# Kernel tuning notes

Measured on AMD Instinct MI355X. Metric: run time of the kernel, lower is better.

Reference implementation:

```python
import jax, jax.numpy as jnp
import numpy as np

SEQ, BATCH, IN, HID = 2048, 64, 256, 256


def setup_inputs() -> dict:
    key = jax.random.key(0)
    ks = jax.random.split(key, 9)
    s_in = 1.0 / np.sqrt(IN)
    s_h = 1.0 / np.sqrt(HID)
    return {
        "x": jax.random.normal(ks[0], (SEQ, BATCH, IN), dtype=jnp.float32),
        "hidden": jnp.zeros((BATCH, HID), dtype=jnp.float32),
        # torch nn.Linear params: weight (out, in), bias (out,)
        "Wz": jax.random.uniform(ks[1], (HID, IN), jnp.float32, -s_in, s_in),
        "bz": jax.random.uniform(ks[2], (HID,), jnp.float32, -s_in, s_in),
        "Uz": jax.random.uniform(ks[3], (HID, HID), jnp.float32, -s_h, s_h),
        "cz": jax.random.uniform(ks[4], (HID,), jnp.float32, -s_h, s_h),
        "Wh": jax.random.uniform(ks[5], (HID, IN), jnp.float32, -s_in, s_in),
        "bh": jax.random.uniform(ks[6], (HID,), jnp.float32, -s_in, s_in),
        "Uh": jax.random.uniform(ks[7], (HID, HID), jnp.float32, -s_h, s_h),
        "ch": jax.random.uniform(ks[8], (HID,), jnp.float32, -s_h, s_h),
    }


def reference(x, hidden, Wz, bz, Uz, cz, Wh, bh, Uh, ch):
    # Precompute all input projections in two batched GEMMs: (S,B,I)@(I,H)
    xz = jnp.einsum("sbi,hi->sbh", x, Wz) + bz  # W_z x_t + b_z
    xh = jnp.einsum("sbi,hi->sbh", x, Wh) + bh  # W_h x_t + b_h

    def step(h, inp):
        xz_t, xh_t = inp
        z = jax.nn.sigmoid(xz_t + h @ Uz.T + cz)
        h_tilde = jnp.tanh(xh_t + h @ Uh.T + ch)
        h_new = (1.0 - z) * h + z * h_tilde
        return h_new, h_new

    h_final, outputs = jax.lax.scan(step, hidden, (xz, xh))
    return outputs, h_final
```

## Files before the change

### kernel.cpp

```cpp
#include <hip/hip_runtime.h>
#include <math.h>

#define SEQ   2048
#define BATCH 64
#define IN    256
#define HID   256
#define NBLK  (SEQ / 8)

typedef _Float16 hf2 __attribute__((ext_vector_type(2)));
typedef _Float16 hf4 __attribute__((ext_vector_type(4)));
typedef _Float16 hf8 __attribute__((ext_vector_type(8)));
typedef float    f32x4 __attribute__((ext_vector_type(4)));

static __device__ __forceinline__ float fast_sigmoid(float x) {
    return __builtin_amdgcn_rcpf(1.0f + __expf(-x));
}

static __device__ __forceinline__ float fast_tanh(float x) {
    const float e = __expf(-2.0f * x);
    return fmaf(2.0f, __builtin_amdgcn_rcpf(1.0f + e), -1.0f);
}

static __device__ __forceinline__ hf8 cvt8(const float4& a, const float4& b) {
    hf8 f;
    f[0] = (_Float16)a.x; f[1] = (_Float16)a.y;
    f[2] = (_Float16)a.z; f[3] = (_Float16)a.w;
    f[4] = (_Float16)b.x; f[5] = (_Float16)b.y;
    f[6] = (_Float16)b.z; f[7] = (_Float16)b.w;
    return f;
}

static __device__ __forceinline__ void bar_lds() {
    asm volatile("s_waitcnt lgkmcnt(0)" ::: "memory");
    __builtin_amdgcn_s_barrier();
}

__global__ __launch_bounds__(256) void w16_kernel(
    const float* __restrict__ Wz, const float* __restrict__ Wh,
    _Float16* __restrict__ W16)
{
    const int idx = blockIdx.x * 256 + threadIdx.x;
    const int row = idx >> 8;
    const int col = idx & 255;
    const float v = (row < 256) ? Wz[row * 256 + col] : Wh[(row - 256) * 256 + col];
    W16[idx] = (_Float16)v;
}

__global__ __launch_bounds__(256) void proj_mfma_kernel(
    const float* __restrict__ x,
    const _Float16* __restrict__ W16,
    const float* __restrict__ bz, const float* __restrict__ cz,
    const float* __restrict__ bh, const float* __restrict__ ch,
    _Float16* __restrict__ xz16,
    float* __restrict__ xh_out)
{
    const int tid  = threadIdx.x;
    const int lane = tid & 63;
    const int w    = tid >> 6;
    const int m0   = blockIdx.x * 16;
    const int col0 = w * 128;

    const int r = lane & 15;
    const int g = lane >> 4;

    f32x4 acc[8] = {f32x4{0,0,0,0}, f32x4{0,0,0,0}, f32x4{0,0,0,0}, f32x4{0,0,0,0},
                    f32x4{0,0,0,0}, f32x4{0,0,0,0}, f32x4{0,0,0,0}, f32x4{0,0,0,0}};

    const float*    xrow  = x   + (size_t)(m0 + r) * IN + g * 8;
    const _Float16* wbase = W16 + (size_t)(col0 + r) * IN + g * 8;

#pragma unroll
    for (int kt = 0; kt < 8; ++kt) {
        const float4 xa = *reinterpret_cast<const float4*>(xrow + kt * 32);
        const float4 xb = *reinterpret_cast<const float4*>(xrow + kt * 32 + 4);
        const hf8 a = cvt8(xa, xb);
#pragma unroll
        for (int t = 0; t < 8; ++t) {
            const hf8 bfrag = *reinterpret_cast<const hf8*>(
                wbase + (size_t)t * 16 * IN + kt * 32);
            acc[t] = __builtin_amdgcn_mfma_f32_16x16x32_f16(a, bfrag, acc[t], 0, 0, 0);
        }
    }

    if (w < 2) {
#pragma unroll
        for (int t = 0; t < 8; ++t) {
            const int c = col0 + t * 16 + r;
            const float bsum = bz[c] + cz[c];
#pragma unroll
            for (int reg = 0; reg < 4; ++reg) {
                const int m = m0 + 4 * g + reg;
                xz16[(size_t)m * HID + c] = (_Float16)(acc[t][reg] + bsum);
            }
        }
    } else {
#pragma unroll
        for (int t = 0; t < 8; ++t) {
            const int c = col0 - 256 + t * 16 + r;
            const float bsum = bh[c] + ch[c];
#pragma unroll
            for (int reg = 0; reg < 4; ++reg) {
                const int m = m0 + 4 * g + reg;
                xh_out[(size_t)m * HID + c] = acc[t][reg] + bsum;
            }
        }
    }
}

__global__ __launch_bounds__(512, 2) void rec_mfma_kernel(
    const float* __restrict__ hidden0,
    const float* __restrict__ Uz,
    const float* __restrict__ Uh,
    const _Float16* __restrict__ xz16,
    float* __restrict__ out,
    float* __restrict__ h_final)
{
    const int b    = blockIdx.x;
    const int tid  = threadIdx.x;
    const int w    = tid >> 6;
    const int lane = tid & 63;
    const int r    = lane & 15;
    const int g    = lane >> 4;

    __shared__ __align__(16) _Float16 hbuf[2][256];
    __shared__ __align__(16) float    sbuf[8][64];
    __shared__ __align__(16) _Float16 xzs[2][8][256];
    __shared__ __align__(16) float    xhs[2][8][256];

    hf8 au[4][8];
    {
        const float* usrc = (r & 1) ? Uh : Uz;
        const int    hrow = r >> 1;
#pragma unroll
        for (int i = 0; i < 4; ++i) {
            const int m = 4 * w + i;
            const float* p0 = usrc + (size_t)(8 * m + hrow) * HID;
#pragma unroll
            for (int kt = 0; kt < 8; ++kt) {
                const float* p = p0 + kt * 32 + 8 * g;
                au[i][kt] = cvt8(*reinterpret_cast<const float4*>(p),
                                 *reinterpret_cast<const float4*>(p + 4));
            }
        }
    }

    if (tid < 256) {
        hbuf[0][tid] = (_Float16)hidden0[b * HID + tid];
    }

    const int o = 32 * w + lane;
    float hp = 0.0f;
    float* pst = out + (size_t)b * HID + o;
    if (lane < 32) {
        hp = hidden0[b * HID + o];
    }

    const int srow = tid >> 6;
    const int scol = (tid & 63) * 4;
    hf4   rz;
    f32x4 rh;
    {
        const size_t a0 = ((size_t)srow * BATCH + b) * HID + scol;
        const hf4   z0 = *reinterpret_cast<const hf4*>(xz16 + a0);
        const f32x4 h0 = *reinterpret_cast<const f32x4*>(out + a0);
        *reinterpret_cast<hf4*>(&xzs[0][srow][scol])   = z0;
        *reinterpret_cast<f32x4*>(&xhs[0][srow][scol]) = h0;
        const size_t a1 = ((size_t)(8 + srow) * BATCH + b) * HID + scol;
        rz = *reinterpret_cast<const hf4*>(xz16 + a1);
        rh = *reinterpret_cast<const f32x4*>(out + a1);
    }
    __syncthreads();

    for (int j = 0; j < NBLK; ++j) {
        const int jb = j & 1;
#pragma unroll
        for (int s = 0; s < 8; ++s) {
            float xzc = 0.0f, xhc = 0.0f;
            if (lane < 32) {
                xzc = (float)xzs[jb][s][o];
                xhc = xhs[jb][s][o];
            }
            hf8 bb[8];
#pragma unroll
            for (int kt = 0; kt < 8; ++kt) {
                bb[kt] = *reinterpret_cast<const hf8*>(
                    &hbuf[s & 1][kt * 32 + 8 * g]);
            }
            f32x4 acc[4] = {f32x4{0,0,0,0}, f32x4{0,0,0,0},
                            f32x4{0,0,0,0}, f32x4{0,0,0,0}};
#pragma unroll
            for (int kt = 0; kt < 8; ++kt) {
#pragma unroll
                for (int i = 0; i < 4; ++i) {
                    acc[i] = __builtin_amdgcn_mfma_f32_16x16x32_f16(
                        au[i][kt], bb[kt], acc[i], 0, 0, 0);
                }
            }
            if (r == 0) {
#pragma unroll
                for (int i = 0; i < 4; ++i) {
                    *reinterpret_cast<f32x4*>(&sbuf[w][i * 16 + g * 4]) = acc[i];
                }
            }
            if (lane < 32) {
                const float2 pr = *reinterpret_cast<const float2*>(
                    &sbuf[w][2 * lane]);
                const float z  = fast_sigmoid(pr.x + xzc);
                const float th = fast_tanh(pr.y + xhc);
                hp = fmaf(z, th - hp, hp);
                *pst = hp;
                pst += (size_t)BATCH * HID;
                hbuf[(s + 1) & 1][o] = (_Float16)hp;
            }
            if (s == 7 && j + 1 < NBLK) {
                *reinterpret_cast<hf4*>(&xzs[jb ^ 1][srow][scol])   = rz;
                *reinterpret_cast<f32x4*>(&xhs[jb ^ 1][srow][scol]) = rh;
                int trow = 8 * (j + 2) + srow;
                if (trow >= SEQ) trow = SEQ - 1;
                const size_t an = ((size_t)trow * BATCH + b) * HID + scol;
                rz = *reinterpret_cast<const hf4*>(xz16 + an);
                rh = *reinterpret_cast<const f32x4*>(out + an);
            }
            bar_lds();
        }
    }

    if (lane < 32) {
        h_final[(size_t)b * HID + o] = hp;
    }
}

extern "C" void kernel_launch(void* const* d_in, const int* in_sizes, int n_in,
                              void* d_out, int out_size, void* d_ws, size_t ws_size,
                              hipStream_t stream) {
    const float* x      = (const float*)d_in[0];
    const float* hidden = (const float*)d_in[1];
    const float* Wz     = (const float*)d_in[2];
    const float* bz     = (const float*)d_in[3];
    const float* Uz     = (const float*)d_in[4];
    const float* cz     = (const float*)d_in[5];
    const float* Wh     = (const float*)d_in[6];
    const float* bh     = (const float*)d_in[7];
    const float* Uh     = (const float*)d_in[8];
    const float* ch     = (const float*)d_in[9];

    float* out     = (float*)d_out;
    float* h_final = out + (size_t)SEQ * BATCH * HID;

    _Float16* xz16 = (_Float16*)d_ws;
    _Float16* W16  = (_Float16*)((char*)d_ws + ((size_t)64 << 20));

    w16_kernel<<<512, 256, 0, stream>>>(Wz, Wh, W16);

    proj_mfma_kernel<<<(SEQ * BATCH) / 16, 256, 0, stream>>>(
        x, W16, bz, cz, bh, ch, xz16, out);

    rec_mfma_kernel<<<BATCH, 512, 0, stream>>>(
        hidden, Uz, Uh, xz16, out, h_final);
}
```

Before: 2.163 ms.

## Split recurrent step across 16 waves with two MFMA tiles each

The recurrent kernel now launches 1024 threads (16 waves) per batch row instead of 512, so each wave owns two 16-row U tiles rather than four. This halves the serial MFMA chain per time step and the per-wave register footprint for the U fragments, and it shortens the critical path of each sequential step. The cost is more waves in each per-step barrier and fewer lanes per wave doing the gate math, which makes barrier synchronisation more expensive.

Result: faster. 2.081 ms (-3.8%).

```diff
diff --git a/kernel.cpp b/kernel.cpp
--- a/kernel.cpp
+++ b/kernel.cpp
@@ -10,6 +10,7 @@
 typedef _Float16 hf2 __attribute__((ext_vector_type(2)));
 typedef _Float16 hf4 __attribute__((ext_vector_type(4)));
 typedef _Float16 hf8 __attribute__((ext_vector_type(8)));
+typedef float    f32x2 __attribute__((ext_vector_type(2)));
 typedef float    f32x4 __attribute__((ext_vector_type(4)));
 
 static __device__ __forceinline__ float fast_sigmoid(float x) {
@@ -107,7 +108,7 @@
     }
 }
 
-__global__ __launch_bounds__(512, 2) void rec_mfma_kernel(
+__global__ __launch_bounds__(1024, 1) void rec_mfma_kernel(
     const float* __restrict__ hidden0,
     const float* __restrict__ Uz,
     const float* __restrict__ Uh,
@@ -123,17 +124,17 @@
     const int g    = lane >> 4;
 
     __shared__ __align__(16) _Float16 hbuf[2][256];
-    __shared__ __align__(16) float    sbuf[8][64];
+    __shared__ __align__(16) float    sbuf[512];
     __shared__ __align__(16) _Float16 xzs[2][8][256];
     __shared__ __align__(16) float    xhs[2][8][256];
 
-    hf8 au[4][8];
+    hf8 au[2][8];
     {
         const float* usrc = (r & 1) ? Uh : Uz;
         const int    hrow = r >> 1;
 #pragma unroll
-        for (int i = 0; i < 4; ++i) {
-            const int m = 4 * w + i;
+        for (int i = 0; i < 2; ++i) {
+            const int m = 2 * w + i;
             const float* p0 = usrc + (size_t)(8 * m + hrow) * HID;
 #pragma unroll
             for (int kt = 0; kt < 8; ++kt) {
@@ -148,26 +149,26 @@
         hbuf[0][tid] = (_Float16)hidden0[b * HID + tid];
     }
 
-    const int o = 32 * w + lane;
+    const int o = 16 * w + (lane & 15);
     float hp = 0.0f;
     float* pst = out + (size_t)b * HID + o;
-    if (lane < 32) {
+    if (lane < 16) {
         hp = hidden0[b * HID + o];
     }
 
-    const int srow = tid >> 6;
-    const int scol = (tid & 63) * 4;
-    hf4   rz;
-    f32x4 rh;
+    const int srow = tid >> 7;
+    const int scol = (tid & 127) * 2;
+    hf2   rz;
+    f32x2 rh;
     {
         const size_t a0 = ((size_t)srow * BATCH + b) * HID + scol;
-        const hf4   z0 = *reinterpret_cast<const hf4*>(xz16 + a0);
-        const f32x4 h0 = *reinterpret_cast<const f32x4*>(out + a0);
-        *reinterpret_cast<hf4*>(&xzs[0][srow][scol])   = z0;
-        *reinterpret_cast<f32x4*>(&xhs[0][srow][scol]) = h0;
+        *reinterpret_cast<hf2*>(&xzs[0][srow][scol]) =
+            *reinterpret_cast<const hf2*>(xz16 + a0);
+        *reinterpret_cast<f32x2*>(&xhs[0][srow][scol]) =
+            *reinterpret_cast<const f32x2*>(out + a0);
         const size_t a1 = ((size_t)(8 + srow) * BATCH + b) * HID + scol;
-        rz = *reinterpret_cast<const hf4*>(xz16 + a1);
-        rh = *reinterpret_cast<const f32x4*>(out + a1);
+        rz = *reinterpret_cast<const hf2*>(xz16 + a1);
+        rh = *reinterpret_cast<const f32x2*>(out + a1);
     }
     __syncthreads();
 
@@ -176,56 +177,47 @@
 #pragma unroll
         for (int s = 0; s < 8; ++s) {
             float xzc = 0.0f, xhc = 0.0f;
-            if (lane < 32) {
+            if (lane < 16) {
                 xzc = (float)xzs[jb][s][o];
                 xhc = xhs[jb][s][o];
             }
-            hf8 bb[8];
+            f32x4 acc0{0, 0, 0, 0}, acc1{0, 0, 0, 0};
 #pragma unroll
             for (int kt = 0; kt < 8; ++kt) {
-                bb[kt] = *reinterpret_cast<const hf8*>(
+                const hf8 bb = *reinterpret_cast<const hf8*>(
                     &hbuf[s & 1][kt * 32 + 8 * g]);
-            }
-            f32x4 acc[4] = {f32x4{0,0,0,0}, f32x4{0,0,0,0},
-                            f32x4{0,0,0,0}, f32x4{0,0,0,0}};
-#pragma unroll
-            for (int kt = 0; kt < 8; ++kt) {
-#pragma unroll
-                for (int i = 0; i < 4; ++i) {
-                    acc[i] = __builtin_amdgcn_mfma_f32_16x16x32_f16(
-                        au[i][kt], bb[kt], acc[i], 0, 0, 0);
-                }
+                acc0 = __builtin_amdgcn_mfma_f32_16x16x32_f16(
+                    au[0][kt], bb, acc0, 0, 0, 0);
+                acc1 = __builtin_amdgcn_mfma_f32_16x16x32_f16(
+                    au[1][kt], bb, acc1, 0, 0, 0);
             }
             if (r == 0) {
-#pragma unroll
-                for (int i = 0; i < 4; ++i) {
-                    *reinterpret_cast<f32x4*>(&sbuf[w][i * 16 + g * 4]) = acc[i];
-                }
-            }
-            if (lane < 32) {
-                const float2 pr = *reinterpret_cast<const float2*>(
-                    &sbuf[w][2 * lane]);
-                const float z  = fast_sigmoid(pr.x + xzc);
-                const float th = fast_tanh(pr.y + xhc);
+                *reinterpret_cast<f32x4*>(&sbuf[(2 * w) * 16 + 4 * g])     = acc0;
+                *reinterpret_cast<f32x4*>(&sbuf[(2 * w + 1) * 16 + 4 * g]) = acc1;
+            }
+            if (lane < 16) {
+                const f32x2 pr = *reinterpret_cast<const f32x2*>(&sbuf[2 * o]);
+                const float z  = fast_sigmoid(pr[0] + xzc);
+                const float th = fast_tanh(pr[1] + xhc);
                 hp = fmaf(z, th - hp, hp);
                 *pst = hp;
                 pst += (size_t)BATCH * HID;
                 hbuf[(s + 1) & 1][o] = (_Float16)hp;
             }
             if (s == 7 && j + 1 < NBLK) {
-                *reinterpret_cast<hf4*>(&xzs[jb ^ 1][srow][scol])   = rz;
-                *reinterpret_cast<f32x4*>(&xhs[jb ^ 1][srow][scol]) = rh;
+                *reinterpret_cast<hf2*>(&xzs[jb ^ 1][srow][scol])   = rz;
+                *reinterpret_cast<f32x2*>(&xhs[jb ^ 1][srow][scol]) = rh;
                 int trow = 8 * (j + 2) + srow;
                 if (trow >= SEQ) trow = SEQ - 1;
                 const size_t an = ((size_t)trow * BATCH + b) * HID + scol;
-                rz = *reinterpret_cast<const hf4*>(xz16 + an);
-                rh = *reinterpret_cast<const f32x4*>(out + an);
+                rz = *reinterpret_cast<const hf2*>(xz16 + an);
+                rh = *reinterpret_cast<const f32x2*>(out + an);
             }
             bar_lds();
         }
     }
 
-    if (lane < 32) {
+    if (lane < 16) {
         h_final[(size_t)b * HID + o] = hp;
     }
 }
@@ -255,6 +247,6 @@
     proj_mfma_kernel<<<(SEQ * BATCH) / 16, 256, 0, stream>>>(
         x, W16, bz, cz, bh, ch, xz16, out);
 
-    rec_mfma_kernel<<<BATCH, 512, 0, stream>>>(
+    rec_mfma_kernel<<<BATCH, 1024, 0, stream>>>(
         hidden, Uz, Uh, xz16, out, h_final);
 }
```
